# Optimization experiments

Hardware: AMD Instinct MI355X
Metric: run time of the kernel (lower is better)

## Reference

```python
import jax, jax.numpy as jnp
import numpy as np

DIM = 1024
HEADS = 16
HEAD_DIM = DIM // HEADS
SCALE = HEAD_DIM ** -0.5
EPS_R = 1e-8
EPS_LN = 1e-5


def setup_inputs() -> dict:
    key = jax.random.key(0)
    ks = jax.random.split(key, 8)
    B, L = 4, 2048
    tokens = jax.random.normal(ks[0], (B, L, DIM), dtype=jnp.float32)
    R = jax.random.uniform(ks[1], (L, L), dtype=jnp.float32)
    s = DIM ** -0.5
    Wq = jax.random.normal(ks[2], (DIM, DIM), dtype=jnp.float32) * s
    Wk = jax.random.normal(ks[3], (DIM, DIM), dtype=jnp.float32) * s
    Wv = jax.random.normal(ks[4], (DIM, DIM), dtype=jnp.float32) * s
    Wp = jax.random.normal(ks[5], (DIM, DIM), dtype=jnp.float32) * s
    beta = jnp.ones((1,), dtype=jnp.float32)
    gamma = jnp.ones((DIM,), dtype=jnp.float32)
    bias = jnp.zeros((DIM,), dtype=jnp.float32)
    return {"tokens": tokens, "R": R, "Wq": Wq, "Wk": Wk, "Wv": Wv,
            "Wp": Wp, "beta": beta, "gamma": gamma, "bias": bias}


def reference(tokens, R, Wq, Wk, Wv, Wp, beta, gamma, bias):
    B, L, D = tokens.shape
    H, Dh = HEADS, HEAD_DIM
    residual = tokens
    # nn.Linear(bias=False): y = x @ W.T
    Q = (tokens @ Wq.T).reshape(B, L, H, Dh).transpose(0, 2, 1, 3)  # [B,H,L,Dh]
    K = (tokens @ Wk.T).reshape(B, L, H, Dh).transpose(0, 2, 1, 3)
    V = (tokens @ Wv.T).reshape(B, L, H, Dh).transpose(0, 2, 1, 3)
    attn = jnp.einsum('bhqd,bhkd->bhqk', Q, K) * SCALE
    log_R = jnp.log(jnp.maximum(R, EPS_R))  # [L,L]
    attn = attn + beta[0] * log_R[None, None, :, :]
    attn = jax.nn.softmax(attn, axis=-1)
    out = jnp.einsum('bhqk,bhkd->bhqd', attn, V)
    out = out.transpose(0, 2, 1, 3).reshape(B, L, D)
    out = out @ Wp.T
    x = out + residual
    mu = jnp.mean(x, axis=-1, keepdims=True)
    var = jnp.mean(jnp.square(x - mu), axis=-1, keepdims=True)
    return (x - mu) * jax.lax.rsqrt(var + EPS_LN) * gamma + bias
```

## Files before the change

kernel.cpp:

```cpp
#include <hip/hip_runtime.h>

#define DEV __device__ __forceinline__

typedef __attribute__((ext_vector_type(2))) float f32x2;
typedef __attribute__((ext_vector_type(4))) float f32x4;
typedef __attribute__((ext_vector_type(16))) float f32x16;
typedef __attribute__((ext_vector_type(8))) short bf8v;
typedef __attribute__((ext_vector_type(4))) unsigned short u16x4;
typedef __attribute__((ext_vector_type(8))) unsigned short u16x8;
typedef __attribute__((ext_vector_type(2))) unsigned int u32x2;
typedef __attribute__((ext_vector_type(4))) unsigned int u32x4;

static constexpr int LSEQ = 2048;
static constexpr int DIM  = 1024;
static constexpr int NH   = 16;
static constexpr int DH   = 64;
static constexpr int NB   = 4;
static constexpr int MROWS = NB * LSEQ;
static constexpr float QSCALE = 0.18033688011112042f;

DEV unsigned short f2bf(float x) {
  unsigned u = __float_as_uint(x);
  return (unsigned short)((u + 0x7fffu + ((u >> 16) & 1u)) >> 16);
}

DEV unsigned cvt_pk_bf16(float a, float b) {
  unsigned r;
  asm("v_cvt_pk_bf16_f32 %0, %1, %2" : "=v"(r) : "v"(a), "v"(b));
  return r;
}

DEV void pl32swap(unsigned& a, unsigned& b) {
  asm("v_permlane32_swap_b32 %0, %1" : "+v"(a), "+v"(b));
}

DEV float fexp2(float x) {
  float r;
  asm("v_exp_f32 %0, %1" : "=v"(r) : "v"(x));
  return r;
}

DEV float max3(float a, float b, float c) { return fmaxf(fmaxf(a, b), c); }

DEV void gload_lds16(const void* g, void* l) {
  __builtin_amdgcn_global_load_lds((const __attribute__((address_space(1))) void*)g,
                                   (__attribute__((address_space(3))) void*)l, 16, 0, 0);
}

__global__ __launch_bounds__(256) void k_prep(
    const float* __restrict__ tokens, unsigned short* __restrict__ tok_bf,
    const float* __restrict__ w0, const float* __restrict__ w1,
    const float* __restrict__ w2, const float* __restrict__ w3,
    unsigned short* __restrict__ wdst,
    const float* __restrict__ R, const float* __restrict__ beta,
    u16x4* __restrict__ rbx) {
  __shared__ u16x4 lds2[2048];
  const int bid = blockIdx.x;
  const int tid = threadIdx.x;
  if (bid < 4096) {
    int i = (bid * 256 + tid) * 8;
    f32x4 a = *(const f32x4*)(tokens + i);
    f32x4 b = *(const f32x4*)(tokens + i + 4);
    u16x8 o;
    o[0] = f2bf(a[0]); o[1] = f2bf(a[1]); o[2] = f2bf(a[2]); o[3] = f2bf(a[3]);
    o[4] = f2bf(b[0]); o[5] = f2bf(b[1]); o[6] = f2bf(b[2]); o[7] = f2bf(b[3]);
    *(u16x8*)(tok_bf + i) = o;
    return;
  }
  if (bid < 6144) {
    int wb = bid - 4096;
    int r = wb >> 9;
    const float* src = (r == 0) ? w0 : (r == 1) ? w1 : (r == 2) ? w2 : w3;
    int i = ((wb & 511) * 256 + tid) * 8;
    f32x4 a = *(const f32x4*)(src + i);
    f32x4 b = *(const f32x4*)(src + i + 4);
    u16x8 o;
    o[0] = f2bf(a[0]); o[1] = f2bf(a[1]); o[2] = f2bf(a[2]); o[3] = f2bf(a[3]);
    o[4] = f2bf(b[0]); o[5] = f2bf(b[1]); o[6] = f2bf(b[2]); o[7] = f2bf(b[3]);
    *(u16x8*)(wdst + (size_t)r * DIM * DIM + i) = o;
    return;
  }
  {
    int rb = bid - 6144;
    const int q0 = (rb & 15) * 128;
    const int t  = rb >> 4;
    const float b = beta[0];
    #pragma unroll
    for (int it = 0; it < 4; ++it) {
      int ql = it * 32 + (tid >> 3);
      int kl = (tid & 7) * 8;
      const float* src = R + (size_t)(q0 + ql) * 2048 + t * 64 + kl;
      f32x4 v0 = *(const f32x4*)src;
      f32x4 v1 = *(const f32x4*)(src + 4);
      u16x4 qa, qb;
      #pragma unroll
      for (int m = 0; m < 4; ++m) {
        qa[m] = f2bf(exp2f(b * log2f(fmaxf(v0[m], 1e-8f))));
        qb[m] = f2bf(exp2f(b * log2f(fmaxf(v1[m], 1e-8f))));
      }
      int s = kl >> 4, w = (kl >> 3) & 1;
      lds2[(((s * 2 + 0) * 128) + ql) * 2 + w] = qa;
      lds2[(((s * 2 + 1) * 128) + ql) * 2 + w] = qb;
    }
    __syncthreads();
    u16x8* O = (u16x8*)rbx;
    #pragma unroll
    for (int j = 0; j < 4; ++j) {
      int f = j * 256 + tid;
      int r = f >> 7, qrel = f & 127;
      O[(size_t)(t * 8 + r) * 2048 + q0 + qrel] = *(const u16x8*)&lds2[(r * 128 + qrel) * 2];
    }
  }
}

DEV void gemm_core(const unsigned short* __restrict__ A, const unsigned short* __restrict__ Bm,
                   int m0, int n0, unsigned short* As, unsigned short* Bs, f32x4 (*acc)[4]) {
  const int tid = threadIdx.x;
  const int lane = tid & 63, wid = tid >> 6;
  const int g = lane >> 4, lq = lane & 15;
  const int wr = wid >> 1, wc = wid & 1;

  int aoff[2][4], boff[2][4];
  #pragma unroll
  for (int kk = 0; kk < 2; ++kk) {
    #pragma unroll
    for (int t = 0; t < 4; ++t) {
      aoff[kk][t] = (((wr * 64 + t * 16 + lq) * 128 + kk * 64 + g * 16) ^ ((lq & 7) << 4));
      boff[kk][t] = (((wc * 64 + t * 16 + lq) * 128 + kk * 64 + g * 16) ^ ((lq & 7) << 4));
    }
  }

  for (int kt = 0; kt < 16; ++kt) {
    #pragma unroll
    for (int i = 0; i < 4; ++i) {
      int chunk = i * 256 + tid;
      int row = chunk >> 3;
      int cc = (chunk & 7) ^ (row & 7);
      gload_lds16(A + (size_t)(m0 + row) * 1024 + kt * 64 + cc * 8, As + (i * 256 + wid * 64) * 8);
      gload_lds16(Bm + (size_t)(n0 + row) * 1024 + kt * 64 + cc * 8, Bs + (i * 256 + wid * 64) * 8);
    }
    __syncthreads();
    #pragma unroll
    for (int kk = 0; kk < 2; ++kk) {
      bf8v af[4], bfr[4];
      #pragma unroll
      for (int mi = 0; mi < 4; ++mi) af[mi] = *(const bf8v*)((const char*)As + aoff[kk][mi]);
      #pragma unroll
      for (int ni = 0; ni < 4; ++ni) bfr[ni] = *(const bf8v*)((const char*)Bs + boff[kk][ni]);
      #pragma unroll
      for (int mi = 0; mi < 4; ++mi)
        #pragma unroll
        for (int ni = 0; ni < 4; ++ni)
          acc[mi][ni] = __builtin_amdgcn_mfma_f32_16x16x32_bf16(af[mi], bfr[ni], acc[mi][ni], 0, 0, 0);
    }
    __syncthreads();
  }
}

__global__ __launch_bounds__(256) void k_gemm_qkv(
    const unsigned short* __restrict__ A, const unsigned short* __restrict__ W,
    unsigned short* __restrict__ Qb, unsigned short* __restrict__ Kb,
    unsigned short* __restrict__ Vt) {
  __shared__ unsigned short As[128 * 64];
  __shared__ unsigned short Bs[128 * 64];
  f32x4 acc[4][4];
  f32x4 z = {0.f, 0.f, 0.f, 0.f};
  #pragma unroll
  for (int mi = 0; mi < 4; ++mi)
    #pragma unroll
    for (int ni = 0; ni < 4; ++ni) acc[mi][ni] = z;

  const int m0 = blockIdx.x * 128, n0 = blockIdx.y * 128;
  gemm_core(A, W, m0, n0, As, Bs, acc);

  const int tid = threadIdx.x;
  const int lane = tid & 63, wid = tid >> 6;
  const int g = lane >> 4, lq = lane & 15;
  const int wr = wid >> 1, wc = wid & 1;
  const int region = n0 >> 10;
  const int nrel0 = n0 & 1023;

  if (region < 2) {
    unsigned short* dst = (region == 0) ? Qb : Kb;
    const float sc = (region == 0) ? QSCALE : 1.0f;
    #pragma unroll
    for (int mi = 0; mi < 4; ++mi)
      #pragma unroll
      for (int ni = 0; ni < 4; ++ni) {
        int m = m0 + wr * 64 + mi * 16 + g * 4;
        int n = nrel0 + wc * 64 + ni * 16 + lq;
        int b = m >> 11, l = m & 2047;
        int h = n >> 6, d = n & 63;
        int base = ((b * NH + h) * LSEQ + l) * DH + d;
        #pragma unroll
        for (int r = 0; r < 4; ++r)
          dst[base + r * DH] = f2bf(acc[mi][ni][r] * sc);
      }
  } else {
    #pragma unroll
    for (int mi = 0; mi < 4; ++mi)
      #pragma unroll
      for (int ni = 0; ni < 4; ++ni) {
        int m = m0 + wr * 64 + mi * 16 + g * 4;
        int n = nrel0 + wc * 64 + ni * 16 + lq;
        int b = m >> 11, l = m & 2047;
        int h = n >> 6, d = n & 63;
        u16x4 pk;
        #pragma unroll
        for (int r = 0; r < 4; ++r) pk[r] = f2bf(acc[mi][ni][r]);
        *(u16x4*)(Vt + (size_t)((b * NH + h) * DH + d) * LSEQ + l) = pk;
      }
  }
}

__global__ __launch_bounds__(256, 4) void k_attn(
    const unsigned short* __restrict__ Qb, const unsigned short* __restrict__ Kb,
    const unsigned short* __restrict__ Vt, const unsigned short* __restrict__ RbX,
    unsigned short* __restrict__ AO) {
  __shared__ unsigned short Ks[2][64 * 64];
  __shared__ unsigned short Vs[2][64 * 64];
  const int tid = threadIdx.x;
  const int lane = tid & 63, wid = tid >> 6;
  const int l32 = lane & 31, hi = lane >> 5;
  int flat = blockIdx.y * 16 + blockIdx.x;
  int nid = (flat & 7) * 128 + (flat >> 3);
  const int bh = nid >> 4;
  const int q0 = (nid & 15) * 128;
  const int b = bh >> 4, h = bh & 15;
  const char* Kbh = (const char*)(Kb + (size_t)bh * LSEQ * DH);
  const char* Vbh = (const char*)(Vt + (size_t)bh * DH * LSEQ);
  const int qw = q0 + wid * 32;
  const int q = qw + l32;

  const unsigned short* Qbh = Qb + (size_t)bh * LSEQ * DH;
  bf8v qf[4];
  #pragma unroll
  for (int s = 0; s < 4; ++s)
    qf[s] = *(const bf8v*)(Qbh + (size_t)q * DH + s * 16 + hi * 8);

  f32x16 oacc[2];
  #pragma unroll
  for (int db = 0; db < 2; ++db)
    #pragma unroll
    for (int r = 0; r < 16; ++r) oacc[db][r] = 0.f;
  float mrun = -__builtin_inff();
  float lrun = 0.f;

  const f32x16 kz = {0.f, 0.f, 0.f, 0.f, 0.f, 0.f, 0.f, 0.f,
                     0.f, 0.f, 0.f, 0.f, 0.f, 0.f, 0.f, 0.f};

  const unsigned rb_off = (unsigned)(hi * 2048 + q) * 16u;
  int koff, voff, ldso;
  {
    int row = tid >> 3;
    int cc = (tid & 7) ^ (row & 7);
    koff = row * (DH * 2) + cc * 16;
    voff = row * (LSEQ * 2) + cc * 16;
    ldso = (wid * 64) * 16;
  }

  gload_lds16(Kbh + koff, (char*)Ks[0] + ldso);
  gload_lds16(Kbh + koff + 4096, (char*)Ks[0] + ldso + 4096);
  gload_lds16(Vbh + voff, (char*)Vs[0] + ldso);
  gload_lds16(Vbh + voff + 131072, (char*)Vs[0] + ldso + 4096);
  __syncthreads();

  auto TILE = [&](int t, int buf, bool pref) {
    const char* rb_t = (const char*)RbX + (size_t)t * 262144;
    u32x4 rrA = *(const u32x4*)(rb_t + rb_off);
    u32x4 rrB = *(const u32x4*)(rb_t + 65536 + rb_off);

    if (pref) {
      const char* Kt = Kbh + (size_t)(t + 1) * (64 * DH * 2);
      const char* Vn = Vbh + (size_t)(t + 1) * (64 * 2);
      gload_lds16(Kt + koff, (char*)Ks[buf ^ 1] + ldso);
      gload_lds16(Kt + koff + 4096, (char*)Ks[buf ^ 1] + ldso + 4096);
      gload_lds16(Vn + voff, (char*)Vs[buf ^ 1] + ldso);
      gload_lds16(Vn + voff + 131072, (char*)Vs[buf ^ 1] + ldso + 4096);
    }

    f32x16 sac[2];
    __builtin_amdgcn_s_setprio(1);
    {
      int r0 = l32, r1 = 32 + l32;
      bf8v kf0 = *(const bf8v*)((const char*)Ks[buf] + ((r0 * 128 + hi * 16) ^ ((r0 & 7) << 4)));
      bf8v kf1 = *(const bf8v*)((const char*)Ks[buf] + ((r1 * 128 + hi * 16) ^ ((r1 & 7) << 4)));
      sac[0] = __builtin_amdgcn_mfma_f32_32x32x16_bf16(kf0, qf[0], kz, 0, 0, 0);
      sac[1] = __builtin_amdgcn_mfma_f32_32x32x16_bf16(kf1, qf[0], kz, 0, 0, 0);
    }
    #pragma unroll
    for (int s = 1; s < 4; ++s) {
      #pragma unroll
      for (int kb2 = 0; kb2 < 2; ++kb2) {
        int row = kb2 * 32 + l32;
        bf8v kf = *(const bf8v*)((const char*)Ks[buf] +
                   ((row * 128 + s * 32 + hi * 16) ^ ((row & 7) << 4)));
        sac[kb2] = __builtin_amdgcn_mfma_f32_32x32x16_bf16(kf, qf[s], sac[kb2], 0, 0, 0);
      }
    }
    __builtin_amdgcn_s_setprio(0);

    float mx;
    {
      float c0 = max3(sac[0][0], sac[0][1], sac[0][2]);
      float c1 = max3(sac[0][4], sac[0][5], sac[0][6]);
      float c2 = max3(sac[0][8], sac[0][9], sac[0][10]);
      float c3 = max3(sac[0][12], sac[0][13], sac[0][14]);
      c0 = max3(c0, sac[0][3], sac[1][0]);
      c1 = max3(c1, sac[0][7], sac[1][4]);
      c2 = max3(c2, sac[0][11], sac[1][8]);
      c3 = max3(c3, sac[0][15], sac[1][12]);
      c0 = max3(c0, sac[1][1], sac[1][2]);
      c1 = max3(c1, sac[1][5], sac[1][6]);
      c2 = max3(c2, sac[1][9], sac[1][10]);
      c3 = max3(c3, sac[1][13], sac[1][14]);
      c0 = max3(c0, sac[1][3], c1);
      c2 = max3(c2, sac[1][7], c3);
      mx = max3(c0, c2, fmaxf(sac[1][11], sac[1][15]));
      mx = fmaxf(mx, __shfl_xor(mx, 32));
    }

    if (__any(mx > mrun + 8.f)) {
      float mnew = fmaxf(mrun, mx);
      float corr = fexp2(mrun - mnew);
      mrun = mnew;
      lrun *= corr;
      #pragma unroll
      for (int db = 0; db < 2; ++db)
        #pragma unroll
        for (int r = 0; r < 16; ++r) oacc[db][r] *= corr;
    }

    f32x2 m2; m2[0] = mrun; m2[1] = mrun;
    f32x2 ls2; ls2[0] = 0.f; ls2[1] = 0.f;

    auto SLICE = [&](int s, const u32x4& rv) {
      const int blk = s >> 1, r0 = 8 * (s & 1);
      unsigned w[4];
      #pragma unroll
      for (int i = 0; i < 4; ++i) {
        f32x2 sv; sv[0] = sac[blk][r0 + 2 * i]; sv[1] = sac[blk][r0 + 2 * i + 1];
        sv = sv - m2;
        f32x2 pe; pe[0] = fexp2(sv[0]); pe[1] = fexp2(sv[1]);
        f32x2 rf;
        rf[0] = __uint_as_float(rv[i] << 16);
        rf[1] = __uint_as_float(rv[i] & 0xffff0000u);
        pe = pe * rf;
        ls2 = ls2 + pe;
        w[i] = cvt_pk_bf16(pe[0], pe[1]);
      }
      pl32swap(w[0], w[2]);
      pl32swap(w[1], w[3]);
      union { unsigned u[4]; bf8v v; } pf;
      pf.u[0] = w[0]; pf.u[1] = w[1]; pf.u[2] = w[2]; pf.u[3] = w[3];
      #pragma unroll
      for (int db = 0; db < 2; ++db) {
        int row = db * 32 + l32;
        bf8v vf = *(const bf8v*)((const char*)Vs[buf] +
                   ((row * 128 + s * 32 + hi * 16) ^ ((row & 7) << 4)));
        oacc[db] = __builtin_amdgcn_mfma_f32_32x32x16_bf16(vf, pf.v, oacc[db], 0, 0, 0);
      }
    };
    SLICE(0, rrA);
    rrA = *(const u32x4*)(rb_t + 131072 + rb_off);
    SLICE(1, rrB);
    rrB = *(const u32x4*)(rb_t + 196608 + rb_off);
    SLICE(2, rrA);
    SLICE(3, rrB);
    lrun += ls2[0] + ls2[1];
    __syncthreads();
  };

  for (int tp = 0; tp < 16; ++tp) {
    TILE(2 * tp,     0, true);
    TILE(2 * tp + 1, 1, tp != 15);
  }

  lrun += __shfl_xor(lrun, 32);
  float inv = 1.f / lrun;
  #pragma unroll
  for (int db = 0; db < 2; ++db)
    #pragma unroll
    for (int u = 0; u < 4; ++u) {
      u32x2 w;
      w[0] = cvt_pk_bf16(oacc[db][4 * u + 0] * inv, oacc[db][4 * u + 1] * inv);
      w[1] = cvt_pk_bf16(oacc[db][4 * u + 2] * inv, oacc[db][4 * u + 3] * inv);
      int d = db * 32 + u * 8 + hi * 4;
      *(u32x2*)(AO + (size_t)(b * LSEQ + q) * DIM + h * DH + d) = w;
    }
}

__global__ __launch_bounds__(256) void k_gemm_proj(
    const unsigned short* __restrict__ A, const unsigned short* __restrict__ W,
    const float* __restrict__ res, float* __restrict__ out) {
  __shared__ unsigned short As[128 * 64];
  __shared__ unsigned short Bs[128 * 64];
  f32x4 acc[4][4];
  f32x4 z = {0.f, 0.f, 0.f, 0.f};
  #pragma unroll
  for (int mi = 0; mi < 4; ++mi)
    #pragma unroll
    for (int ni = 0; ni < 4; ++ni) acc[mi][ni] = z;

  const int m0 = blockIdx.x * 128, n0 = blockIdx.y * 128;
  gemm_core(A, W, m0, n0, As, Bs, acc);

  const int tid = threadIdx.x;
  const int lane = tid & 63, wid = tid >> 6;
  const int g = lane >> 4, lq = lane & 15;
  const int wr = wid >> 1, wc = wid & 1;
  #pragma unroll
  for (int mi = 0; mi < 4; ++mi)
    #pragma unroll
    for (int ni = 0; ni < 4; ++ni) {
      int m = m0 + wr * 64 + mi * 16 + g * 4;
      int n = n0 + wc * 64 + ni * 16 + lq;
      #pragma unroll
      for (int r = 0; r < 4; ++r) {
        int idx = (m + r) * 1024 + n;
        out[idx] = acc[mi][ni][r] + res[idx];
      }
    }
}

__global__ __launch_bounds__(256) void k_ln(float* __restrict__ x,
                                            const float* __restrict__ gamma,
                                            const float* __restrict__ bias) {
  const int row = blockIdx.x;
  const int tid = threadIdx.x;
  float* xr = x + (size_t)row * 1024;
  f32x4 v = *(f32x4*)(xr + tid * 4);
  float s = v[0] + v[1] + v[2] + v[3];
  float ss = v[0] * v[0] + v[1] * v[1] + v[2] * v[2] + v[3] * v[3];
  #pragma unroll
  for (int off = 1; off < 64; off <<= 1) {
    s += __shfl_xor(s, off);
    ss += __shfl_xor(ss, off);
  }
  __shared__ float red[8];
  const int lane = tid & 63, wid = tid >> 6;
  if (lane == 0) { red[wid] = s; red[wid + 4] = ss; }
  __syncthreads();
  s = red[0] + red[1] + red[2] + red[3];
  ss = red[4] + red[5] + red[6] + red[7];
  float mu = s * (1.f / 1024.f);
  float var = ss * (1.f / 1024.f) - mu * mu;
  float rs = rsqrtf(var + 1e-5f);
  f32x4 gm = *(const f32x4*)(gamma + tid * 4);
  f32x4 bi = *(const f32x4*)(bias + tid * 4);
  f32x4 o;
  #pragma unroll
  for (int j = 0; j < 4; ++j) o[j] = (v[j] - mu) * rs * gm[j] + bi[j];
  *(f32x4*)(xr + tid * 4) = o;
}

extern "C" void kernel_launch(void* const* d_in, const int* in_sizes, int n_in,
                              void* d_out, int out_size, void* d_ws, size_t ws_size,
                              hipStream_t stream) {
  const float* tokens = (const float*)d_in[0];
  const float* R      = (const float*)d_in[1];
  const float* Wq     = (const float*)d_in[2];
  const float* Wk     = (const float*)d_in[3];
  const float* Wv     = (const float*)d_in[4];
  const float* Wp     = (const float*)d_in[5];
  const float* beta   = (const float*)d_in[6];
  const float* gamma  = (const float*)d_in[7];
  const float* bias   = (const float*)d_in[8];
  float* out = (float*)d_out;
  char* ws = (char*)d_ws;

  unsigned short* tok_bf = (unsigned short*)(ws);
  unsigned short* wqkv   = (unsigned short*)(ws + 16777216);
  u16x4*          rbx    = (u16x4*)(ws + 25165824);
  unsigned short* qb     = (unsigned short*)(ws + 41943040);
  unsigned short* kb     = (unsigned short*)(ws + 58720256);
  unsigned short* vt     = (unsigned short*)(ws + 75497472);
  unsigned short* wp     = wqkv + 3 * DIM * DIM;
  unsigned short* ao     = tok_bf;

  k_prep<<<6656, 256, 0, stream>>>(tokens, tok_bf, Wq, Wk, Wv, Wp, wqkv, R, beta, rbx);

  k_gemm_qkv<<<dim3(64, 24), 256, 0, stream>>>(tok_bf, wqkv, qb, kb, vt);
  k_attn<<<dim3(16, 64), 256, 0, stream>>>(qb, kb, vt, (const unsigned short*)rbx, ao);
  k_gemm_proj<<<dim3(64, 8), 256, 0, stream>>>(ao, wp, tokens, out);
  k_ln<<<8192, 256, 0, stream>>>(out, gamma, bias);
}
```

Before: 229.9 us.

## Pre-tile K and V in MFMA fragment order to make attention loads contiguous

The QKV GEMM epilogue now writes K and V into a tiled layout of 64-key blocks, arranged so each lane's MFMA operand fragment is a contiguous 16-byte chunk. The attention kernel then copies each 8 KB tile to LDS with linear, fully coalesced loads and reads fragments at fixed offsets. This drops the XOR swizzle address math and the strided V-transposed global loads. The trade-off is more scattered 2-byte stores for K in the GEMM epilogue, and possible LDS bank conflicts now that the swizzle is gone.

```diff
diff --git a/kernel.cpp b/kernel.cpp
--- a/kernel.cpp
+++ b/kernel.cpp
@@ -159,8 +159,8 @@
 
 __global__ __launch_bounds__(256) void k_gemm_qkv(
     const unsigned short* __restrict__ A, const unsigned short* __restrict__ W,
-    unsigned short* __restrict__ Qb, unsigned short* __restrict__ Kb,
-    unsigned short* __restrict__ Vt) {
+    unsigned short* __restrict__ Qb, unsigned short* __restrict__ KX,
+    unsigned short* __restrict__ VX) {
   __shared__ unsigned short As[128 * 64];
   __shared__ unsigned short Bs[128 * 64];
   f32x4 acc[4][4];
@@ -180,9 +180,7 @@
   const int region = n0 >> 10;
   const int nrel0 = n0 & 1023;
 
-  if (region < 2) {
-    unsigned short* dst = (region == 0) ? Qb : Kb;
-    const float sc = (region == 0) ? QSCALE : 1.0f;
+  if (region == 0) {
     #pragma unroll
     for (int mi = 0; mi < 4; ++mi)
       #pragma unroll
@@ -194,7 +192,22 @@
         int base = ((b * NH + h) * LSEQ + l) * DH + d;
         #pragma unroll
         for (int r = 0; r < 4; ++r)
-          dst[base + r * DH] = f2bf(acc[mi][ni][r] * sc);
+          Qb[base + r * DH] = f2bf(acc[mi][ni][r] * QSCALE);
+      }
+  } else if (region == 1) {
+    #pragma unroll
+    for (int mi = 0; mi < 4; ++mi)
+      #pragma unroll
+      for (int ni = 0; ni < 4; ++ni) {
+        int m = m0 + wr * 64 + mi * 16 + g * 4;
+        int n = nrel0 + wc * 64 + ni * 16 + lq;
+        int b = m >> 11, l = m & 2047;
+        int h = n >> 6, d = n & 63;
+        size_t base = (size_t)(b * NH + h) * 131072 + (l >> 6) * 4096 +
+                      (d >> 3) * 512 + (l & 63) * 8 + (d & 7);
+        #pragma unroll
+        for (int r = 0; r < 4; ++r)
+          KX[base + r * 8] = f2bf(acc[mi][ni][r]);
       }
   } else {
     #pragma unroll
@@ -208,14 +221,16 @@
         u16x4 pk;
         #pragma unroll
         for (int r = 0; r < 4; ++r) pk[r] = f2bf(acc[mi][ni][r]);
-        *(u16x4*)(Vt + (size_t)((b * NH + h) * DH + d) * LSEQ + l) = pk;
+        size_t idx = (size_t)(b * NH + h) * 131072 + (l >> 6) * 4096 +
+                     ((l >> 3) & 7) * 512 + d * 8 + (l & 7);
+        *(u16x4*)(VX + idx) = pk;
       }
   }
 }
 
 __global__ __launch_bounds__(256, 4) void k_attn(
-    const unsigned short* __restrict__ Qb, const unsigned short* __restrict__ Kb,
-    const unsigned short* __restrict__ Vt, const unsigned short* __restrict__ RbX,
+    const unsigned short* __restrict__ Qb, const unsigned short* __restrict__ KX,
+    const unsigned short* __restrict__ VX, const unsigned short* __restrict__ RbX,
     unsigned short* __restrict__ AO) {
   __shared__ unsigned short Ks[2][64 * 64];
   __shared__ unsigned short Vs[2][64 * 64];
@@ -227,8 +242,8 @@
   const int bh = nid >> 4;
   const int q0 = (nid & 15) * 128;
   const int b = bh >> 4, h = bh & 15;
-  const char* Kbh = (const char*)(Kb + (size_t)bh * LSEQ * DH);
-  const char* Vbh = (const char*)(Vt + (size_t)bh * DH * LSEQ);
+  const char* Kbh = (const char*)KX + (size_t)bh * 262144;
+  const char* Vbh = (const char*)VX + (size_t)bh * 262144;
   const int qw = q0 + wid * 32;
   const int q = qw + l32;
 
@@ -250,19 +265,13 @@
                      0.f, 0.f, 0.f, 0.f, 0.f, 0.f, 0.f, 0.f};
 
   const unsigned rb_off = (unsigned)(hi * 2048 + q) * 16u;
-  int koff, voff, ldso;
-  {
-    int row = tid >> 3;
-    int cc = (tid & 7) ^ (row & 7);
-    koff = row * (DH * 2) + cc * 16;
-    voff = row * (LSEQ * 2) + cc * 16;
-    ldso = (wid * 64) * 16;
-  }
-
-  gload_lds16(Kbh + koff, (char*)Ks[0] + ldso);
-  gload_lds16(Kbh + koff + 4096, (char*)Ks[0] + ldso + 4096);
-  gload_lds16(Vbh + voff, (char*)Vs[0] + ldso);
-  gload_lds16(Vbh + voff + 131072, (char*)Vs[0] + ldso + 4096);
+  const int soff = tid * 16;
+  const int fbase = hi * 1024 + l32 * 16;
+
+  gload_lds16(Kbh + soff, (char*)Ks[0] + soff);
+  gload_lds16(Kbh + 4096 + soff, (char*)Ks[0] + 4096 + soff);
+  gload_lds16(Vbh + soff, (char*)Vs[0] + soff);
+  gload_lds16(Vbh + 4096 + soff, (char*)Vs[0] + 4096 + soff);
   __syncthreads();
 
   auto TILE = [&](int t, int buf, bool pref) {
@@ -271,32 +280,23 @@
     u32x4 rrB = *(const u32x4*)(rb_t + 65536 + rb_off);
 
     if (pref) {
-      const char* Kt = Kbh + (size_t)(t + 1) * (64 * DH * 2);
-      const char* Vn = Vbh + (size_t)(t + 1) * (64 * 2);
-      gload_lds16(Kt + koff, (char*)Ks[buf ^ 1] + ldso);
-      gload_lds16(Kt + koff + 4096, (char*)Ks[buf ^ 1] + ldso + 4096);
-      gload_lds16(Vn + voff, (char*)Vs[buf ^ 1] + ldso);
-      gload_lds16(Vn + voff + 131072, (char*)Vs[buf ^ 1] + ldso + 4096);
-    }
-
+      const char* Kt = Kbh + (size_t)(t + 1) * 8192;
+      const char* Vn = Vbh + (size_t)(t + 1) * 8192;
+      gload_lds16(Kt + soff, (char*)Ks[buf ^ 1] + soff);
+      gload_lds16(Kt + 4096 + soff, (char*)Ks[buf ^ 1] + 4096 + soff);
+      gload_lds16(Vn + soff, (char*)Vs[buf ^ 1] + soff);
+      gload_lds16(Vn + 4096 + soff, (char*)Vs[buf ^ 1] + 4096 + soff);
+    }
+
+    const char* kb_ = (const char*)Ks[buf] + fbase;
     f32x16 sac[2];
     __builtin_amdgcn_s_setprio(1);
-    {
-      int r0 = l32, r1 = 32 + l32;
-      bf8v kf0 = *(const bf8v*)((const char*)Ks[buf] + ((r0 * 128 + hi * 16) ^ ((r0 & 7) << 4)));
-      bf8v kf1 = *(const bf8v*)((const char*)Ks[buf] + ((r1 * 128 + hi * 16) ^ ((r1 & 7) << 4)));
-      sac[0] = __builtin_amdgcn_mfma_f32_32x32x16_bf16(kf0, qf[0], kz, 0, 0, 0);
-      sac[1] = __builtin_amdgcn_mfma_f32_32x32x16_bf16(kf1, qf[0], kz, 0, 0, 0);
-    }
+    sac[0] = __builtin_amdgcn_mfma_f32_32x32x16_bf16(*(const bf8v*)(kb_), qf[0], kz, 0, 0, 0);
+    sac[1] = __builtin_amdgcn_mfma_f32_32x32x16_bf16(*(const bf8v*)(kb_ + 512), qf[0], kz, 0, 0, 0);
     #pragma unroll
     for (int s = 1; s < 4; ++s) {
-      #pragma unroll
-      for (int kb2 = 0; kb2 < 2; ++kb2) {
-        int row = kb2 * 32 + l32;
-        bf8v kf = *(const bf8v*)((const char*)Ks[buf] +
-                   ((row * 128 + s * 32 + hi * 16) ^ ((row & 7) << 4)));
-        sac[kb2] = __builtin_amdgcn_mfma_f32_32x32x16_bf16(kf, qf[s], sac[kb2], 0, 0, 0);
-      }
+      sac[0] = __builtin_amdgcn_mfma_f32_32x32x16_bf16(*(const bf8v*)(kb_ + s * 2048), qf[s], sac[0], 0, 0, 0);
+      sac[1] = __builtin_amdgcn_mfma_f32_32x32x16_bf16(*(const bf8v*)(kb_ + s * 2048 + 512), qf[s], sac[1], 0, 0, 0);
     }
     __builtin_amdgcn_s_setprio(0);
 
@@ -333,6 +333,7 @@
 
     f32x2 m2; m2[0] = mrun; m2[1] = mrun;
     f32x2 ls2; ls2[0] = 0.f; ls2[1] = 0.f;
+    const char* vb_ = (const char*)Vs[buf] + fbase;
 
     auto SLICE = [&](int s, const u32x4& rv) {
       const int blk = s >> 1, r0 = 8 * (s & 1);
@@ -353,13 +354,8 @@
       pl32swap(w[1], w[3]);
       union { unsigned u[4]; bf8v v; } pf;
       pf.u[0] = w[0]; pf.u[1] = w[1]; pf.u[2] = w[2]; pf.u[3] = w[3];
-      #pragma unroll
-      for (int db = 0; db < 2; ++db) {
-        int row = db * 32 + l32;
-        bf8v vf = *(const bf8v*)((const char*)Vs[buf] +
-                   ((row * 128 + s * 32 + hi * 16) ^ ((row & 7) << 4)));
-        oacc[db] = __builtin_amdgcn_mfma_f32_32x32x16_bf16(vf, pf.v, oacc[db], 0, 0, 0);
-      }
+      oacc[0] = __builtin_amdgcn_mfma_f32_32x32x16_bf16(*(const bf8v*)(vb_ + s * 2048), pf.v, oacc[0], 0, 0, 0);
+      oacc[1] = __builtin_amdgcn_mfma_f32_32x32x16_bf16(*(const bf8v*)(vb_ + s * 2048 + 512), pf.v, oacc[1], 0, 0, 0);
     };
     SLICE(0, rrA);
     rrA = *(const u32x4*)(rb_t + 131072 + rb_off);
@@ -473,15 +469,15 @@
   unsigned short* wqkv   = (unsigned short*)(ws + 16777216);
   u16x4*          rbx    = (u16x4*)(ws + 25165824);
   unsigned short* qb     = (unsigned short*)(ws + 41943040);
-  unsigned short* kb     = (unsigned short*)(ws + 58720256);
-  unsigned short* vt     = (unsigned short*)(ws + 75497472);
+  unsigned short* kx     = (unsigned short*)(ws + 58720256);
+  unsigned short* vx     = (unsigned short*)(ws + 75497472);
   unsigned short* wp     = wqkv + 3 * DIM * DIM;
   unsigned short* ao     = tok_bf;
 
   k_prep<<<6656, 256, 0, stream>>>(tokens, tok_bf, Wq, Wk, Wv, Wp, wqkv, R, beta, rbx);
 
-  k_gemm_qkv<<<dim3(64, 24), 256, 0, stream>>>(tok_bf, wqkv, qb, kb, vt);
-  k_attn<<<dim3(16, 64), 256, 0, stream>>>(qb, kb, vt, (const unsigned short*)rbx, ao);
+  k_gemm_qkv<<<dim3(64, 24), 256, 0, stream>>>(tok_bf, wqkv, qb, kx, vx);
+  k_attn<<<dim3(16, 64), 256, 0, stream>>>(qb, kx, vx, (const unsigned short*)rbx, ao);
   k_gemm_proj<<<dim3(64, 8), 256, 0, stream>>>(ao, wp, tokens, out);
   k_ln<<<8192, 256, 0, stream>>>(out, gamma, bias);
 }
```

After: 280.3 us. 21.9% more time.
